# Kernel optimization log

Measured on AMD Instinct MI355X. Metric: run time of the kernel, lower is better.

## Reference

```python
import jax, jax.numpy as jnp
import numpy as np

B, C, H, W = 8, 16, 256, 256
D = C - 4  # hidden channels
N = H * W


def _grid_edges(h, w):
    idx = np.arange(h * w).reshape(h, w)
    right = np.stack([idx[:, :-1].ravel(), idx[:, 1:].ravel()])
    down = np.stack([idx[:-1, :].ravel(), idx[1:, :].ravel()])
    e = np.concatenate([right, down], axis=1)
    # both directions (undirected 4-neighborhood)
    return np.concatenate([e, e[::-1]], axis=1).astype(np.int64)


def setup_inputs() -> dict:
    key = jax.random.key(0)
    ks = jax.random.split(key, 12)
    s = lambda *sh: 1.0 / np.sqrt(np.prod(sh[1:]))
    inp = {
        "x": jax.random.normal(ks[0], (B, C, H, W), jnp.float32),
        "edge_index": jnp.asarray(_grid_edges(H, W)),
        "steps": 8,
        # hidden_update: Conv2d(D, D, 3, padding=1)
        "Wh": jax.random.normal(ks[1], (D, D, 3, 3), jnp.float32) * s(D, D * 9),
        "bh": jnp.zeros((D,), jnp.float32),
        # graph message passing linear (D -> D)
        "Wmp": jax.random.normal(ks[2], (D, D), jnp.float32) * s(D, D),
        "bmp": jnp.zeros((D,), jnp.float32),
        # alive_update: Conv2d(D, 1, 1)
        "Wa": jax.random.normal(ks[3], (1, D), jnp.float32) * s(1, D),
        "ba": jnp.zeros((1,), jnp.float32),
        # rgb_decode: Conv2d(D+1, D, 1) -> ReLU -> Conv2d(D, 3, 1)
        "Wr1": jax.random.normal(ks[4], (D, D + 1), jnp.float32) * s(D, D + 1),
        "br1": jnp.zeros((D,), jnp.float32),
        "Wr2": jax.random.normal(ks[5], (3, D), jnp.float32) * s(3, D),
        "br2": jnp.zeros((3,), jnp.float32),
    }
    return inp


def _conv1x1(x, w, b):
    # x: [B,Ci,H,W], w: [Co,Ci]
    return jnp.einsum("bchw,oc->bohw", x, w) + b[None, :, None, None]


def _graph_mp(hidden, edge_index, Wmp, bmp, deg_inv):
    # hidden: [B,D,H,W] -> nodes [B,N,D]
    b, d, h, w = hidden.shape
    nodes = hidden.reshape(b, d, h * w).transpose(0, 2, 1)
    src, dst = edge_index[0], edge_index[1]
    msg = nodes[:, src] @ Wmp.T + bmp  # [B,E,D]
    agg = jnp.zeros_like(nodes).at[:, dst].add(msg)  # scatter-add
    agg = agg * deg_inv[None, :, None]  # mean aggregation
    return agg.transpose(0, 2, 1).reshape(b, d, h, w)


def reference(x, edge_index, steps, Wh, bh, Wmp, bmp, Wa, ba, Wr1, br1, Wr2, br2):
    n = x.shape[2] * x.shape[3]
    deg = jnp.zeros((n,), x.dtype).at[edge_index[1]].add(1.0)
    deg_inv = 1.0 / jnp.maximum(deg, 1.0)
    for _ in range(steps):
        hidden = x[:, 4:]
        h_local = jax.lax.conv_general_dilated(
            hidden, Wh, (1, 1), ((1, 1), (1, 1)),
            dimension_numbers=("NCHW", "OIHW", "NCHW"),
        ) + bh[None, :, None, None]
        h_graph = _graph_mp(hidden, edge_index, Wmp, bmp, deg_inv)
        hidden_new = jax.nn.elu(hidden + h_local + h_graph)
        alive_new = jax.nn.sigmoid(_conv1x1(hidden_new, Wa, ba))
        cat = jnp.concatenate([hidden_new, alive_new], axis=1)
        rgb_new = jax.nn.sigmoid(_conv1x1(jax.nn.relu(_conv1x1(cat, Wr1, br1)), Wr2, br2))
        rgb_new = rgb_new * alive_new
        x = jnp.concatenate([alive_new, rgb_new, hidden_new], axis=1)
    return x
```

## Files before the change

### kernel.cpp

```cpp
#include <hip/hip_runtime.h>
#include <math.h>

#define Wd 256
#define Hd 256
#define Nd (Wd*Hd)
#define Dd 12
#define Bd 8

__global__ __launch_bounds__(512, 4) void nca_step(
    const float* __restrict__ src, long src_batch_stride, long src_off,
    float* __restrict__ dst,
    const float* __restrict__ Wh, const float* __restrict__ bh,
    const float* __restrict__ Wmp, const float* __restrict__ bmp)
{
    __shared__ float tile[12 * 34 * 36];
    __shared__ float wts[12 * 12 * 12];

    const int tid = threadIdx.x;
    const int bx = blockIdx.x, by = blockIdx.y, b = blockIdx.z;
    const int x0t = bx * 32, y0t = by * 32;
    const float* sp = src + (long)b * src_batch_stride + src_off;

    for (int idx = tid; idx < 12 * 12 * 12; idx += 512) {
        int i = idx / 144; int rem = idx % 144; int o = rem / 12; int k = rem % 12;
        float v = 0.0f;
        if (k < 9) {
            v = Wh[(o * 12 + i) * 9 + k];
            if (k == 4 && o == i) v += 1.0f;
        } else if (k == 9) {
            v = Wmp[o * 12 + i];
        }
        wts[idx] = v;
    }

    for (int idx = tid; idx < 12 * 34 * 34; idx += 512) {
        int c = idx / 1156; int rem = idx % 1156; int ly = rem / 34; int lx = rem % 34;
        int gy = y0t + ly - 1, gx = x0t + lx - 1;
        float v = 0.0f;
        if (gy >= 0 && gy < Hd && gx >= 0 && gx < Wd)
            v = sp[(long)c * Nd + gy * Wd + gx];
        tile[c * 1224 + ly * 36 + lx] = v;
    }
    __syncthreads();

    const int tx = tid & 15, ty = tid >> 4;
    const int px0 = tx * 2;
    const int py = ty;
    const int gx0 = x0t + px0, gy = y0t + py;

    float dinv[2];
    #pragma unroll
    for (int p = 0; p < 2; ++p) {
        int gx = gx0 + p;
        int deg = (gx > 0) + (gx < Wd - 1) + (gy > 0) + (gy < Hd - 1);
        dinv[p] = 1.0f / (float)deg;
    }

    float acc[2][12];
    #pragma unroll
    for (int o = 0; o < 12; ++o) {
        float bv = bh[o] + bmp[o];
        acc[0][o] = bv; acc[1][o] = bv;
    }

    #pragma unroll
    for (int i = 0; i < 12; ++i) {
        const float* tp = &tile[i * 1224 + py * 36 + px0];
        float t0[4], t1[4], t2[4];
        #pragma unroll
        for (int c = 0; c < 4; ++c) {
            t0[c] = tp[c]; t1[c] = tp[36 + c]; t2[c] = tp[72 + c];
        }
        float ns[2];
        #pragma unroll
        for (int p = 0; p < 2; ++p)
            ns[p] = (t0[p + 1] + t2[p + 1] + t1[p] + t1[p + 2]) * dinv[p];

        const float* wp = &wts[i * 144];
        #pragma unroll
        for (int o = 0; o < 12; ++o) {
            const float* w = wp + o * 12;
            float w0 = w[0], w1 = w[1], w2 = w[2], w3 = w[3], w4 = w[4];
            float w5 = w[5], w6 = w[6], w7 = w[7], w8 = w[8], w9 = w[9];
            #pragma unroll
            for (int p = 0; p < 2; ++p) {
                float a = acc[p][o];
                a = fmaf(w0, t0[p],     a);
                a = fmaf(w1, t0[p + 1], a);
                a = fmaf(w2, t0[p + 2], a);
                a = fmaf(w3, t1[p],     a);
                a = fmaf(w4, t1[p + 1], a);
                a = fmaf(w5, t1[p + 2], a);
                a = fmaf(w6, t2[p],     a);
                a = fmaf(w7, t2[p + 1], a);
                a = fmaf(w8, t2[p + 2], a);
                a = fmaf(w9, ns[p],     a);
                acc[p][o] = a;
            }
        }
    }

    float* dp = dst + (long)b * (12 * (long)Nd);
    #pragma unroll
    for (int o = 0; o < 12; ++o) {
        float e[2];
        #pragma unroll
        for (int p = 0; p < 2; ++p) {
            float a = acc[p][o];
            e[p] = a > 0.0f ? a : (__expf(a) - 1.0f);
        }
        *(float2*)&dp[(long)o * Nd + gy * Wd + gx0] = make_float2(e[0], e[1]);
    }
}

__global__ __launch_bounds__(256) void nca_final(
    const float* __restrict__ hsrc, float* __restrict__ out,
    const float* __restrict__ Wa, const float* __restrict__ ba,
    const float* __restrict__ Wr1, const float* __restrict__ br1,
    const float* __restrict__ Wr2, const float* __restrict__ br2)
{
    int p = blockIdx.x * 256 + threadIdx.x;
    int b = blockIdx.y;
    const float* hp = hsrc + (long)b * 12 * Nd + p;
    float h[12];
    #pragma unroll
    for (int c = 0; c < 12; ++c) h[c] = hp[(long)c * Nd];

    float za = ba[0];
    #pragma unroll
    for (int c = 0; c < 12; ++c) za = fmaf(Wa[c], h[c], za);
    float alive = 1.0f / (1.0f + __expf(-za));

    float r1[12];
    #pragma unroll
    for (int o = 0; o < 12; ++o) {
        float z = br1[o];
        #pragma unroll
        for (int c = 0; c < 12; ++c) z = fmaf(Wr1[o * 13 + c], h[c], z);
        z = fmaf(Wr1[o * 13 + 12], alive, z);
        r1[o] = fmaxf(z, 0.0f);
    }

    float* op = out + (long)b * 16 * Nd + p;
    op[0] = alive;
    #pragma unroll
    for (int j = 0; j < 3; ++j) {
        float z = br2[j];
        #pragma unroll
        for (int o = 0; o < 12; ++o) z = fmaf(Wr2[j * 12 + o], r1[o], z);
        op[(long)(1 + j) * Nd] = (1.0f / (1.0f + __expf(-z))) * alive;
    }
    #pragma unroll
    for (int c = 0; c < 12; ++c) op[(long)(4 + c) * Nd] = h[c];
}

extern "C" void kernel_launch(void* const* d_in, const int* in_sizes, int n_in,
                              void* d_out, int out_size, void* d_ws, size_t ws_size,
                              hipStream_t stream) {
    const float* x   = (const float*)d_in[0];
    const float* Wh  = (const float*)d_in[3];
    const float* bh  = (const float*)d_in[4];
    const float* Wmp = (const float*)d_in[5];
    const float* bmp = (const float*)d_in[6];
    const float* Wa  = (const float*)d_in[7];
    const float* ba  = (const float*)d_in[8];
    const float* Wr1 = (const float*)d_in[9];
    const float* br1 = (const float*)d_in[10];
    const float* Wr2 = (const float*)d_in[11];
    const float* br2 = (const float*)d_in[12];

    float* bufA = (float*)d_out;
    float* bufB = (float*)d_ws;

    dim3 grid(8, 8, 8), block(512);
    nca_step<<<grid, block, 0, stream>>>(x,    (long)16 * Nd, (long)4 * Nd, bufA, Wh, bh, Wmp, bmp);
    nca_step<<<grid, block, 0, stream>>>(bufA, (long)12 * Nd, 0,            bufB, Wh, bh, Wmp, bmp);
    nca_step<<<grid, block, 0, stream>>>(bufB, (long)12 * Nd, 0,            bufA, Wh, bh, Wmp, bmp);
    nca_step<<<grid, block, 0, stream>>>(bufA, (long)12 * Nd, 0,            bufB, Wh, bh, Wmp, bmp);
    nca_step<<<grid, block, 0, stream>>>(bufB, (long)12 * Nd, 0,            bufA, Wh, bh, Wmp, bmp);
    nca_step<<<grid, block, 0, stream>>>(bufA, (long)12 * Nd, 0,            bufB, Wh, bh, Wmp, bmp);
    nca_step<<<grid, block, 0, stream>>>(bufB, (long)12 * Nd, 0,            bufA, Wh, bh, Wmp, bmp);
    nca_step<<<grid, block, 0, stream>>>(bufA, (long)12 * Nd, 0,            bufB, Wh, bh, Wmp, bmp);
    nca_final<<<dim3(Nd / 256, Bd), block.x == 512 ? dim3(256) : dim3(256), 0, stream>>>(
        bufB, (float*)d_out, Wa, ba, Wr1, br1, Wr2, br2);
}
```

Measured before the change: 424.6 us.

## Precompute weight table once and remap NCA step to one pixel per thread

```diff
diff --git a/kernel.cpp b/kernel.cpp
--- a/kernel.cpp
+++ b/kernel.cpp
@@ -4,25 +4,16 @@
 #define Wd 256
 #define Hd 256
 #define Nd (Wd*Hd)
-#define Dd 12
 #define Bd 8
 
-__global__ __launch_bounds__(512, 4) void nca_step(
-    const float* __restrict__ src, long src_batch_stride, long src_off,
-    float* __restrict__ dst,
+__global__ __launch_bounds__(256) void nca_prep(
     const float* __restrict__ Wh, const float* __restrict__ bh,
-    const float* __restrict__ Wmp, const float* __restrict__ bmp)
+    const float* __restrict__ Wmp, const float* __restrict__ bmp,
+    float* __restrict__ wtab)
 {
-    __shared__ float tile[12 * 34 * 36];
-    __shared__ float wts[12 * 12 * 12];
-
-    const int tid = threadIdx.x;
-    const int bx = blockIdx.x, by = blockIdx.y, b = blockIdx.z;
-    const int x0t = bx * 32, y0t = by * 32;
-    const float* sp = src + (long)b * src_batch_stride + src_off;
-
-    for (int idx = tid; idx < 12 * 12 * 12; idx += 512) {
-        int i = idx / 144; int rem = idx % 144; int o = rem / 12; int k = rem % 12;
+    int idx = blockIdx.x * 256 + threadIdx.x;
+    if (idx < 1728) {
+        int i = idx / 144, rem = idx % 144, o = rem / 12, k = rem % 12;
         float v = 0.0f;
         if (k < 9) {
             v = Wh[(o * 12 + i) * 9 + k];
@@ -30,86 +21,87 @@
         } else if (k == 9) {
             v = Wmp[o * 12 + i];
         }
-        wts[idx] = v;
+        wtab[idx] = v;
+    } else if (idx < 1740) {
+        int o = idx - 1728;
+        wtab[idx] = bh[o] + bmp[o];
     }
+}
 
-    for (int idx = tid; idx < 12 * 34 * 34; idx += 512) {
-        int c = idx / 1156; int rem = idx % 1156; int ly = rem / 34; int lx = rem % 34;
-        int gy = y0t + ly - 1, gx = x0t + lx - 1;
-        float v = 0.0f;
-        if (gy >= 0 && gy < Hd && gx >= 0 && gx < Wd)
-            v = sp[(long)c * Nd + gy * Wd + gx];
-        tile[c * 1224 + ly * 36 + lx] = v;
+__global__ __launch_bounds__(512, 4) void nca_step(
+    const float* __restrict__ src, long sbs, long soff,
+    float* __restrict__ dst, const float* __restrict__ wtab)
+{
+    __shared__ float tile[12 * 648];
+
+    const int tid = threadIdx.x;
+    const int bx = blockIdx.x, by = blockIdx.y, b = blockIdx.z;
+    const int x0 = bx * 32, y0 = by * 16;
+    const float* sp = src + (long)b * sbs + soff;
+
+    const int pr0 = tid / 34, pc0 = tid % 34;
+    const int gy0s = y0 + pr0 - 1, gx0s = x0 + pc0 - 1;
+    const bool in0 = (unsigned)gy0s < 256u && (unsigned)gx0s < 256u;
+    const long go0 = (long)gy0s * Wd + gx0s;
+    const int lo0 = pr0 * 36 + pc0;
+
+    const int p1 = tid + 512;
+    const int pr1 = p1 / 34, pc1 = p1 % 34;
+    const int gy1s = y0 + pr1 - 1, gx1s = x0 + pc1 - 1;
+    const bool v1 = p1 < 612;
+    const bool in1 = v1 && (unsigned)gy1s < 256u && (unsigned)gx1s < 256u;
+    const long go1 = (long)gy1s * Wd + gx1s;
+    const int lo1 = pr1 * 36 + pc1;
+
+    #pragma unroll
+    for (int c = 0; c < 12; ++c) {
+        float a0 = in0 ? sp[(long)c * Nd + go0] : 0.0f;
+        tile[c * 648 + lo0] = a0;
+        if (v1) {
+            float a1 = in1 ? sp[(long)c * Nd + go1] : 0.0f;
+            tile[c * 648 + lo1] = a1;
+        }
     }
     __syncthreads();
 
-    const int tx = tid & 15, ty = tid >> 4;
-    const int px0 = tx * 2;
-    const int py = ty;
-    const int gx0 = x0t + px0, gy = y0t + py;
+    const int tx = tid & 31, ty = tid >> 5;
+    const int gx = x0 + tx, gy = y0 + ty;
+    const int deg = (gx > 0) + (gx < Wd - 1) + (gy > 0) + (gy < Hd - 1);
+    const float dinv = 1.0f / (float)deg;
 
-    float dinv[2];
+    const float* bias = wtab + 1728;
+    float acc[12];
     #pragma unroll
-    for (int p = 0; p < 2; ++p) {
-        int gx = gx0 + p;
-        int deg = (gx > 0) + (gx < Wd - 1) + (gy > 0) + (gy < Hd - 1);
-        dinv[p] = 1.0f / (float)deg;
-    }
-
-    float acc[2][12];
-    #pragma unroll
-    for (int o = 0; o < 12; ++o) {
-        float bv = bh[o] + bmp[o];
-        acc[0][o] = bv; acc[1][o] = bv;
-    }
+    for (int o = 0; o < 12; ++o) acc[o] = bias[o];
 
     #pragma unroll
     for (int i = 0; i < 12; ++i) {
-        const float* tp = &tile[i * 1224 + py * 36 + px0];
-        float t0[4], t1[4], t2[4];
-        #pragma unroll
-        for (int c = 0; c < 4; ++c) {
-            t0[c] = tp[c]; t1[c] = tp[36 + c]; t2[c] = tp[72 + c];
-        }
-        float ns[2];
-        #pragma unroll
-        for (int p = 0; p < 2; ++p)
-            ns[p] = (t0[p + 1] + t2[p + 1] + t1[p] + t1[p + 2]) * dinv[p];
+        const float* tp = &tile[i * 648 + ty * 36 + tx];
+        float t00 = tp[0],  t01 = tp[1],  t02 = tp[2];
+        float t10 = tp[36], t11 = tp[37], t12 = tp[38];
+        float t20 = tp[72], t21 = tp[73], t22 = tp[74];
+        float ns = (t01 + t21 + t10 + t12) * dinv;
 
-        const float* wp = &wts[i * 144];
+        const float4* w4 = (const float4*)(wtab + (long)i * 144);
         #pragma unroll
         for (int o = 0; o < 12; ++o) {
-            const float* w = wp + o * 12;
-            float w0 = w[0], w1 = w[1], w2 = w[2], w3 = w[3], w4 = w[4];
-            float w5 = w[5], w6 = w[6], w7 = w[7], w8 = w[8], w9 = w[9];
-            #pragma unroll
-            for (int p = 0; p < 2; ++p) {
-                float a = acc[p][o];
-                a = fmaf(w0, t0[p],     a);
-                a = fmaf(w1, t0[p + 1], a);
-                a = fmaf(w2, t0[p + 2], a);
-                a = fmaf(w3, t1[p],     a);
-                a = fmaf(w4, t1[p + 1], a);
-                a = fmaf(w5, t1[p + 2], a);
-                a = fmaf(w6, t2[p],     a);
-                a = fmaf(w7, t2[p + 1], a);
-                a = fmaf(w8, t2[p + 2], a);
-                a = fmaf(w9, ns[p],     a);
-                acc[p][o] = a;
-            }
+            float4 wa = w4[o * 3 + 0];
+            float4 wb = w4[o * 3 + 1];
+            float4 wc = w4[o * 3 + 2];
+            float a = acc[o];
+            a = fmaf(wa.x, t00, a); a = fmaf(wa.y, t01, a); a = fmaf(wa.z, t02, a);
+            a = fmaf(wa.w, t10, a); a = fmaf(wb.x, t11, a); a = fmaf(wb.y, t12, a);
+            a = fmaf(wb.z, t20, a); a = fmaf(wb.w, t21, a); a = fmaf(wc.x, t22, a);
+            a = fmaf(wc.y, ns, a);
+            acc[o] = a;
         }
     }
 
-    float* dp = dst + (long)b * (12 * (long)Nd);
+    float* dp = dst + (long)b * (12L * Nd) + (long)gy * Wd + gx;
     #pragma unroll
     for (int o = 0; o < 12; ++o) {
-        float e[2];
-        #pragma unroll
-        for (int p = 0; p < 2; ++p) {
-            float a = acc[p][o];
-            e[p] = a > 0.0f ? a : (__expf(a) - 1.0f);
-        }
-        *(float2*)&dp[(long)o * Nd + gy * Wd + gx0] = make_float2(e[0], e[1]);
+        float a = acc[o];
+        dp[(long)o * Nd] = a > 0.0f ? a : (__expf(a) - 1.0f);
     }
 }
 
@@ -171,16 +163,19 @@
 
     float* bufA = (float*)d_out;
     float* bufB = (float*)d_ws;
+    float* wtab = (float*)d_out + 12L * Nd * Bd;
 
-    dim3 grid(8, 8, 8), block(512);
-    nca_step<<<grid, block, 0, stream>>>(x,    (long)16 * Nd, (long)4 * Nd, bufA, Wh, bh, Wmp, bmp);
-    nca_step<<<grid, block, 0, stream>>>(bufA, (long)12 * Nd, 0,            bufB, Wh, bh, Wmp, bmp);
-    nca_step<<<grid, block, 0, stream>>>(bufB, (long)12 * Nd, 0,            bufA, Wh, bh, Wmp, bmp);
-    nca_step<<<grid, block, 0, stream>>>(bufA, (long)12 * Nd, 0,            bufB, Wh, bh, Wmp, bmp);
-    nca_step<<<grid, block, 0, stream>>>(bufB, (long)12 * Nd, 0,            bufA, Wh, bh, Wmp, bmp);
-    nca_step<<<grid, block, 0, stream>>>(bufA, (long)12 * Nd, 0,            bufB, Wh, bh, Wmp, bmp);
-    nca_step<<<grid, block, 0, stream>>>(bufB, (long)12 * Nd, 0,            bufA, Wh, bh, Wmp, bmp);
-    nca_step<<<grid, block, 0, stream>>>(bufA, (long)12 * Nd, 0,            bufB, Wh, bh, Wmp, bmp);
-    nca_final<<<dim3(Nd / 256, Bd), block.x == 512 ? dim3(256) : dim3(256), 0, stream>>>(
-        bufB, (float*)d_out, Wa, ba, Wr1, br1, Wr2, br2);
+    nca_prep<<<dim3(7), dim3(256), 0, stream>>>(Wh, bh, Wmp, bmp, wtab);
+
+    dim3 grid(8, 16, 8), block(512);
+    nca_step<<<grid, block, 0, stream>>>(x,    (long)16 * Nd, (long)4 * Nd, bufA, wtab);
+    nca_step<<<grid, block, 0, stream>>>(bufA, (long)12 * Nd, 0,            bufB, wtab);
+    nca_step<<<grid, block, 0, stream>>>(bufB, (long)12 * Nd, 0,            bufA, wtab);
+    nca_step<<<grid, block, 0, stream>>>(bufA, (long)12 * Nd, 0,            bufB, wtab);
+    nca_step<<<grid, block, 0, stream>>>(bufB, (long)12 * Nd, 0,            bufA, wtab);
+    nca_step<<<grid, block, 0, stream>>>(bufA, (long)12 * Nd, 0,            bufB, wtab);
+    nca_step<<<grid, block, 0, stream>>>(bufB, (long)12 * Nd, 0,            bufA, wtab);
+    nca_step<<<grid, block, 0, stream>>>(bufA, (long)12 * Nd, 0,            bufB, wtab);
+    nca_final<<<dim3(Nd / 256, Bd), dim3(256), 0, stream>>>(bufB, (float*)d_out,
+                                                            Wa, ba, Wr1, br1, Wr2, br2);
 }
```

Result: slower. 508.3 us (+19.7%).
